# Optimization experiments

Hardware: AMD Instinct MI355X
Metric: run time of the kernel (lower is better)

Reference implementation:

```python
import jax, jax.numpy as jnp
import numpy as np
import math

B, S, H, K = 512, 200, 256, 16

def setup_inputs() -> dict:
    key = jax.random.key(0)
    ks = jax.random.split(key, 8)
    scale = 1.0 / math.sqrt(H)
    return {
        "input_tensor": jax.random.normal(ks[0], (B, S, H), dtype=jnp.float32),
        "item_mask": jax.random.randint(ks[1], (B, S, 1), 0, 2) > 0,
        "time_f_w_matrix": jax.random.uniform(ks[2], (B, S, 1), dtype=jnp.float32),
        "W1": jax.random.normal(ks[3], (H, H), dtype=jnp.float32) * scale,
        "b1": jnp.zeros((H,), dtype=jnp.float32),
        "W2": jax.random.normal(ks[4], (H, H), dtype=jnp.float32) * scale,
        "b2": jnp.zeros((H,), dtype=jnp.float32),
        "W3": jax.random.normal(ks[5], (H, K), dtype=jnp.float32) * scale,
    }

def reference(input_tensor, item_mask, time_f_w_matrix, W1, b1, W2, b2, W3):
    # small MLP: two Linear+ReLU then bias-free Linear to k_interests
    h = jax.nn.relu(jnp.einsum('bsh,hd->bsd', input_tensor, W1) + b1)
    h = jax.nn.relu(jnp.einsum('bsh,hd->bsd', h, W2) + b2)
    D = jnp.einsum('bsh,hk->bsk', h, W3)              # [B,S,K]
    D = jax.nn.softmax(D, axis=-1)                    # softmax over interests
    mask = item_mask[:, :, 0:1]                       # [B,S,1] bool, broadcast over K
    D = jnp.where(mask, D, jnp.float32(-10000.0))
    D = D / jnp.float32(math.sqrt(K))
    D = jax.nn.softmax(D, axis=-2)                    # softmax over sequence
    D = time_f_w_matrix[:, :, 0:1] * D                # time weighting
    # einsum 'nij,nik->nkj': pool items into K interest vectors
    return jnp.einsum('bsh,bsk->bkh', input_tensor, D)
```

## Files before the change

### kernel.cpp

```cpp
#include <hip/hip_runtime.h>
#include <math.h>

#define HDIM 256
#define KDIM 16
#define SDIM 200
#define BDIM 512
#define NROWS (BDIM * SDIM)
#define TM 32

typedef __bf16 bf16x8 __attribute__((ext_vector_type(8)));
typedef __bf16 bf16x4 __attribute__((ext_vector_type(4)));
typedef float  f32x4  __attribute__((ext_vector_type(4)));

__global__ __launch_bounds__(256) void pack_w_kernel(
    const float* __restrict__ src, __bf16* __restrict__ hi,
    __bf16* __restrict__ lo, int lgN)
{
    int idx = blockIdx.x * 256 + threadIdx.x;
    int N = 1 << lgN;
    int k = idx >> lgN;
    int n = idx & (N - 1);
    float v = src[idx];
    __bf16 h = (__bf16)v;
    float r = v - (float)h;
    int d = (((k >> 3) << lgN) + n) * 8 + (k & 7);
    hi[d] = h;
    lo[d] = (__bf16)r;
}

__global__ __launch_bounds__(256, 4) void mlp_softk_mfma(
    const float* __restrict__ X, const int* __restrict__ mask,
    const __bf16* __restrict__ W1h, const __bf16* __restrict__ W1l,
    const float* __restrict__ b1,
    const __bf16* __restrict__ W2h, const __bf16* __restrict__ W2l,
    const float* __restrict__ b2,
    const __bf16* __restrict__ W3h, const __bf16* __restrict__ W3l,
    float* __restrict__ P)
{
    __shared__ __bf16 Ahi[TM * HDIM];
    __shared__ __bf16 Alo[TM * HDIM];

    const int tid  = threadIdx.x;
    const int lane = tid & 63;
    const int w    = tid >> 6;
    const int l15  = lane & 15;
    const int quad = lane >> 4;
    const long r0  = (long)blockIdx.x * TM;

    {
        const float4* Xt = (const float4*)(X + r0 * HDIM);
        #pragma unroll
        for (int t = 0; t < (TM * HDIM / 4) / 256; ++t) {
            int v4  = tid + t * 256;
            float4 f = Xt[v4];
            int row = v4 >> 6;
            int col = (v4 & 63) << 2;
            int kgs = (col >> 3) ^ (row & 31);
            int base = row * HDIM + kgs * 8 + (col & 7);
            __bf16 h0 = (__bf16)f.x, h1 = (__bf16)f.y,
                   h2 = (__bf16)f.z, h3 = (__bf16)f.w;
            bf16x4 hv = {h0, h1, h2, h3};
            bf16x4 lv = {(__bf16)(f.x - (float)h0), (__bf16)(f.y - (float)h1),
                         (__bf16)(f.z - (float)h2), (__bf16)(f.w - (float)h3)};
            *(bf16x4*)(&Ahi[base]) = hv;
            *(bf16x4*)(&Alo[base]) = lv;
        }
    }
    __syncthreads();

    f32x4 acc[2][4];

    auto layer = [&](const __bf16* __restrict__ Wh, const __bf16* __restrict__ Wl,
                     const float* __restrict__ bias) {
        #pragma unroll
        for (int mt = 0; mt < 2; ++mt)
            #pragma unroll
            for (int nt = 0; nt < 4; ++nt)
                acc[mt][nt] = (f32x4){0.f, 0.f, 0.f, 0.f};

        #pragma unroll 2
        for (int kc = 0; kc < 8; ++kc) {
            bf16x8 bh[4], bl[4], ah[2], al[2];
            #pragma unroll
            for (int nt = 0; nt < 4; ++nt) {
                int n  = w * 64 + nt * 16 + l15;
                int kg = kc * 4 + quad;
                bh[nt] = *(const bf16x8*)(Wh + (kg * HDIM + n) * 8);
                bl[nt] = *(const bf16x8*)(Wl + (kg * HDIM + n) * 8);
            }
            #pragma unroll
            for (int mt = 0; mt < 2; ++mt) {
                int row = mt * 16 + l15;
                int kgs = (kc * 4 + quad) ^ (row & 31);
                ah[mt] = *(const bf16x8*)(&Ahi[row * HDIM + kgs * 8]);
                al[mt] = *(const bf16x8*)(&Alo[row * HDIM + kgs * 8]);
            }
            #pragma unroll
            for (int mt = 0; mt < 2; ++mt)
                #pragma unroll
                for (int nt = 0; nt < 4; ++nt) {
                    acc[mt][nt] = __builtin_amdgcn_mfma_f32_16x16x32_bf16(
                        ah[mt], bh[nt], acc[mt][nt], 0, 0, 0);
                    acc[mt][nt] = __builtin_amdgcn_mfma_f32_16x16x32_bf16(
                        al[mt], bh[nt], acc[mt][nt], 0, 0, 0);
                    acc[mt][nt] = __builtin_amdgcn_mfma_f32_16x16x32_bf16(
                        ah[mt], bl[nt], acc[mt][nt], 0, 0, 0);
                }
        }
        __syncthreads();

        float bias_v[4];
        #pragma unroll
        for (int nt = 0; nt < 4; ++nt) bias_v[nt] = bias[w * 64 + nt * 16 + l15];
        #pragma unroll
        for (int mt = 0; mt < 2; ++mt)
            #pragma unroll
            for (int nt = 0; nt < 4; ++nt)
                #pragma unroll
                for (int r = 0; r < 4; ++r) {
                    float v = fmaxf(acc[mt][nt][r] + bias_v[nt], 0.f);
                    int row = mt * 16 + quad * 4 + r;
                    int col = w * 64 + nt * 16 + l15;
                    int idx = row * HDIM + (((col >> 3) ^ (row & 31)) * 8) + (col & 7);
                    __bf16 h = (__bf16)v;
                    Ahi[idx] = h;
                    Alo[idx] = (__bf16)(v - (float)h);
                }
        __syncthreads();
    };

    layer(W1h, W1l, b1);
    layer(W2h, W2l, b2);

    if (w < 2) {
        f32x4 lg = {0.f, 0.f, 0.f, 0.f};
        #pragma unroll
        for (int kc = 0; kc < 8; ++kc) {
            int row = w * 16 + l15;
            int kg  = kc * 4 + quad;
            int kgs = kg ^ (row & 31);
            bf16x8 ah = *(const bf16x8*)(&Ahi[row * HDIM + kgs * 8]);
            bf16x8 al = *(const bf16x8*)(&Alo[row * HDIM + kgs * 8]);
            bf16x8 bh = *(const bf16x8*)(W3h + (kg * KDIM + l15) * 8);
            bf16x8 bl = *(const bf16x8*)(W3l + (kg * KDIM + l15) * 8);
            lg = __builtin_amdgcn_mfma_f32_16x16x32_bf16(ah, bh, lg, 0, 0, 0);
            lg = __builtin_amdgcn_mfma_f32_16x16x32_bf16(al, bh, lg, 0, 0, 0);
            lg = __builtin_amdgcn_mfma_f32_16x16x32_bf16(ah, bl, lg, 0, 0, 0);
        }

        #pragma unroll
        for (int r = 0; r < 4; ++r) {
            float v  = lg[r];
            float mx = v;
            mx = fmaxf(mx, __shfl_xor(mx, 1));
            mx = fmaxf(mx, __shfl_xor(mx, 2));
            mx = fmaxf(mx, __shfl_xor(mx, 4));
            mx = fmaxf(mx, __shfl_xor(mx, 8));
            float e = __expf(v - mx);
            float s = e;
            s += __shfl_xor(s, 1);
            s += __shfl_xor(s, 2);
            s += __shfl_xor(s, 4);
            s += __shfl_xor(s, 8);
            int grow = (int)r0 + w * 16 + quad * 4 + r;
            int mv   = mask[grow];
            float ov = mv ? (e / s) * 0.25f : -2500.0f;
            P[(long)grow * KDIM + l15] = ov;
        }
    }
}

__global__ __launch_bounds__(256) void softs_agg_kernel(
    const float* __restrict__ X, const float* __restrict__ tf,
    const float* __restrict__ P, float* __restrict__ out)
{
    __shared__ float wl[SDIM * KDIM];
    __shared__ float tfl[SDIM];
    __shared__ float psum[256];
    __shared__ float invk[KDIM];
    __shared__ float red[KDIM * HDIM];

    const int tid = threadIdx.x;
    const int b   = blockIdx.x;

    const float* Pb = P + (long)b * SDIM * KDIM;
    float ps = 0.f;
    #pragma unroll
    for (int t = 0; t < 13; ++t) {
        int i = tid + t * 256;
        if (i < SDIM * KDIM) {
            float e = __expf(Pb[i]);
            wl[i] = e;
            ps += e;
        }
    }
    psum[tid] = ps;
    if (tid < SDIM) tfl[tid] = tf[b * SDIM + tid];
    __syncthreads();

    if (tid < KDIM) {
        float s = 0.f;
        #pragma unroll
        for (int g = 0; g < 16; ++g) s += psum[tid + g * 16];
        invk[tid] = 1.f / s;
    }
    __syncthreads();

    #pragma unroll
    for (int t = 0; t < 13; ++t) {
        int i = tid + t * 256;
        if (i < SDIM * KDIM) wl[i] *= tfl[i >> 4] * invk[i & 15];
    }
    __syncthreads();

    const int wv = tid >> 6;
    const int sh = wv >> 1;
    const int hh = wv & 1;
    const int ln = tid & 63;

    float accx[KDIM], accy[KDIM];
    #pragma unroll
    for (int k = 0; k < KDIM; ++k) { accx[k] = 0.f; accy[k] = 0.f; }

    const float2* Xb  = (const float2*)(X + (long)b * SDIM * HDIM) + hh * 64 + ln;
    const f32x4*  wl4 = (const f32x4*)wl;
    const int s0 = sh * 100;
    #pragma unroll 4
    for (int si = 0; si < 100; ++si) {
        int s = s0 + si;
        float2 x = Xb[(long)s * (HDIM / 2)];
        f32x4 d0 = wl4[s * 4 + 0];
        f32x4 d1 = wl4[s * 4 + 1];
        f32x4 d2 = wl4[s * 4 + 2];
        f32x4 d3 = wl4[s * 4 + 3];
        #pragma unroll
        for (int j = 0; j < 4; ++j) {
            accx[0 + j]  = fmaf(x.x, d0[j], accx[0 + j]);
            accx[4 + j]  = fmaf(x.x, d1[j], accx[4 + j]);
            accx[8 + j]  = fmaf(x.x, d2[j], accx[8 + j]);
            accx[12 + j] = fmaf(x.x, d3[j], accx[12 + j]);
            accy[0 + j]  = fmaf(x.y, d0[j], accy[0 + j]);
            accy[4 + j]  = fmaf(x.y, d1[j], accy[4 + j]);
            accy[8 + j]  = fmaf(x.y, d2[j], accy[8 + j]);
            accy[12 + j] = fmaf(x.y, d3[j], accy[12 + j]);
        }
    }

    if (sh == 1) {
        #pragma unroll
        for (int k = 0; k < KDIM; ++k) {
            red[k * HDIM + hh * 128 + 2 * ln + 0] = accx[k];
            red[k * HDIM + hh * 128 + 2 * ln + 1] = accy[k];
        }
    }
    __syncthreads();
    if (sh == 0) {
        float* ob = out + (long)b * KDIM * HDIM + hh * 128 + 2 * ln;
        #pragma unroll
        for (int k = 0; k < KDIM; ++k) {
            float2 o;
            o.x = accx[k] + red[k * HDIM + hh * 128 + 2 * ln + 0];
            o.y = accy[k] + red[k * HDIM + hh * 128 + 2 * ln + 1];
            *(float2*)(ob + (long)k * HDIM) = o;
        }
    }
}

extern "C" void kernel_launch(void* const* d_in, const int* in_sizes, int n_in,
                              void* d_out, int out_size, void* d_ws, size_t ws_size,
                              hipStream_t stream) {
    (void)in_sizes; (void)n_in; (void)out_size; (void)ws_size;
    const float* X    = (const float*)d_in[0];
    const int*   mask = (const int*)  d_in[1];
    const float* tf   = (const float*)d_in[2];
    const float* W1   = (const float*)d_in[3];
    const float* b1   = (const float*)d_in[4];
    const float* W2   = (const float*)d_in[5];
    const float* b2   = (const float*)d_in[6];
    const float* W3   = (const float*)d_in[7];
    float* out = (float*)d_out;

    char* ws = (char*)d_ws;
    float*  P   = (float*)ws;
    __bf16* w1h = (__bf16*)(ws + 6553600);
    __bf16* w1l = w1h + 65536;
    __bf16* w2h = w1l + 65536;
    __bf16* w2l = w2h + 65536;
    __bf16* w3h = w2l + 65536;
    __bf16* w3l = w3h + 4096;

    pack_w_kernel<<<256, 256, 0, stream>>>(W1, w1h, w1l, 8);
    pack_w_kernel<<<256, 256, 0, stream>>>(W2, w2h, w2l, 8);
    pack_w_kernel<<<16,  256, 0, stream>>>(W3, w3h, w3l, 4);
    mlp_softk_mfma<<<NROWS / TM, 256, 0, stream>>>(X, mask, w1h, w1l, b1,
                                                   w2h, w2l, b2, w3h, w3l, P);
    softs_agg_kernel<<<BDIM, 256, 0, stream>>>(X, tf, P, out);
}
```

Baseline: 285.2 us.

## Merge weight-pack launches, fully unroll K loop, drop occupancy hint

Folds the three weight-packing launches into one kernel that indexes by destination, so the bf16 hi/lo stores are coalesced and two launches disappear. Fully unrolls the 8-step K-chunk loop in each MLP layer and removes the min-blocks-per-SM launch bound on the MFMA kernel. More unrolling and the relaxed bound can raise register use and lower occupancy in exchange for fewer loop overheads and better load scheduling.

```diff
diff --git a/kernel.cpp b/kernel.cpp
--- a/kernel.cpp
+++ b/kernel.cpp
@@ -12,23 +12,33 @@
 typedef __bf16 bf16x4 __attribute__((ext_vector_type(4)));
 typedef float  f32x4  __attribute__((ext_vector_type(4)));
 
-__global__ __launch_bounds__(256) void pack_w_kernel(
-    const float* __restrict__ src, __bf16* __restrict__ hi,
-    __bf16* __restrict__ lo, int lgN)
+__global__ __launch_bounds__(256) void pack_all(
+    const float* __restrict__ W1, const float* __restrict__ W2,
+    const float* __restrict__ W3,
+    __bf16* __restrict__ w1h, __bf16* __restrict__ w1l,
+    __bf16* __restrict__ w2h, __bf16* __restrict__ w2l,
+    __bf16* __restrict__ w3h, __bf16* __restrict__ w3l)
 {
-    int idx = blockIdx.x * 256 + threadIdx.x;
-    int N = 1 << lgN;
-    int k = idx >> lgN;
-    int n = idx & (N - 1);
-    float v = src[idx];
+    int gid = blockIdx.x * 256 + threadIdx.x;
+    const float* src;
+    __bf16 *oh, *ol;
+    int e, N;
+    if (gid < 65536)       { src = W1; oh = w1h; ol = w1l; e = gid;          N = 256; }
+    else if (gid < 131072) { src = W2; oh = w2h; ol = w2l; e = gid - 65536;  N = 256; }
+    else if (gid < 135168) { src = W3; oh = w3h; ol = w3l; e = gid - 131072; N = 16;  }
+    else return;
+
+    int j  = e & 7;
+    int n  = (e >> 3) & (N - 1);
+    int kg = e >> 3; kg = (N == 256) ? (kg >> 8) : (kg >> 4);
+    int k  = kg * 8 + j;
+    float v = src[k * N + n];
     __bf16 h = (__bf16)v;
-    float r = v - (float)h;
-    int d = (((k >> 3) << lgN) + n) * 8 + (k & 7);
-    hi[d] = h;
-    lo[d] = (__bf16)r;
+    oh[e] = h;
+    ol[e] = (__bf16)(v - (float)h);
 }
 
-__global__ __launch_bounds__(256, 4) void mlp_softk_mfma(
+__global__ __launch_bounds__(256) void mlp_softk_mfma(
     const float* __restrict__ X, const int* __restrict__ mask,
     const __bf16* __restrict__ W1h, const __bf16* __restrict__ W1l,
     const float* __restrict__ b1,
@@ -78,7 +88,7 @@
             for (int nt = 0; nt < 4; ++nt)
                 acc[mt][nt] = (f32x4){0.f, 0.f, 0.f, 0.f};
 
-        #pragma unroll 2
+        #pragma unroll
         for (int kc = 0; kc < 8; ++kc) {
             bf16x8 bh[4], bl[4], ah[2], al[2];
             #pragma unroll
@@ -289,9 +299,7 @@
     __bf16* w3h = w2l + 65536;
     __bf16* w3l = w3h + 4096;
 
-    pack_w_kernel<<<256, 256, 0, stream>>>(W1, w1h, w1l, 8);
-    pack_w_kernel<<<256, 256, 0, stream>>>(W2, w2h, w2l, 8);
-    pack_w_kernel<<<16,  256, 0, stream>>>(W3, w3h, w3l, 4);
+    pack_all<<<528, 256, 0, stream>>>(W1, W2, W3, w1h, w1l, w2h, w2l, w3h, w3l);
     mlp_softk_mfma<<<NROWS / TM, 256, 0, stream>>>(X, mask, w1h, w1l, b1,
                                                    w2h, w2l, b2, w3h, w3l, P);
     softs_agg_kernel<<<BDIM, 256, 0, stream>>>(X, tf, P, out);
```

Measured after the change: 263.6 us. 1.08x faster.
